# Kernel optimization log

Measured on AMD Instinct MI355X. Metric: run time of the kernel, lower is better.

The kernel has to match this reference:

```python
import jax, jax.numpy as jnp
import numpy as np

B, S, F, DK = 4, 2048, 1024, 1024

def setup_inputs() -> dict:
    key = jax.random.key(0)
    ks = jax.random.split(key, 9)
    sF = 1.0 / np.sqrt(F)
    sD = 1.0 / np.sqrt(DK)
    return {
        "x":  jax.random.normal(ks[0], (B, S, F), dtype=jnp.float32),
        "Wq": jax.random.normal(ks[1], (DK, F), dtype=jnp.float32) * sF,
        "bq": jax.random.normal(ks[2], (DK,), dtype=jnp.float32) * sF,
        "Wk": jax.random.normal(ks[3], (DK, F), dtype=jnp.float32) * sF,
        "bk": jax.random.normal(ks[4], (DK,), dtype=jnp.float32) * sF,
        "Wv": jax.random.normal(ks[5], (DK, F), dtype=jnp.float32) * sF,
        "bv": jax.random.normal(ks[6], (DK,), dtype=jnp.float32) * sF,
        "Wo": jax.random.normal(ks[7], (F, DK), dtype=jnp.float32) * sD,
        "bo": jax.random.normal(ks[8], (F,), dtype=jnp.float32) * sD,
    }

def reference(x, Wq, bq, Wk, bk, Wv, bv, Wo, bo):
    # Linear layers (torch convention: y = x @ W.T + b)
    q = jnp.einsum('bsf,df->bsd', x, Wq) + bq  # (B,S,DK)
    k = jnp.einsum('bsf,df->bsd', x, Wk) + bk  # (B,S,DK)
    v = jnp.einsum('bsf,df->bsd', x, Wv) + bv  # (B,S,DK)
    scale = 1.0 / (q.shape[-1] ** 0.5)
    scores = jnp.einsum('bqd,bkd->bqk', q, k) * scale  # (B,Sq,Sk)
    # Faithful to original: softmax over dim=-2 (the QUERY axis)
    attn = jax.nn.softmax(scores, axis=-2)
    ctx = jnp.einsum('bqk,bkd->bqd', attn, v)  # (B,S,DK)
    out = jnp.einsum('bsd,fd->bsf', ctx, Wo) + bo  # (B,S,F)
    return out
```

## Files before the change

### kernel.cpp

```cpp
#include <hip/hip_runtime.h>
#include <hip/hip_bf16.h>
#include <math.h>

typedef __bf16 bf16_t;
typedef __bf16 bf16x8 __attribute__((ext_vector_type(8)));
typedef float f32x4 __attribute__((ext_vector_type(4)));


__device__ __forceinline__ void g2l16(const bf16_t* g, bf16_t* l) {
  __builtin_amdgcn_global_load_lds(
      (const __attribute__((address_space(1))) void*)g,
      (__attribute__((address_space(3))) void*)l, 16, 0, 0);
}

__device__ __forceinline__ float waveMax(float v) {
#pragma unroll
  for (int o = 32; o > 0; o >>= 1) v = fmaxf(v, __shfl_xor(v, o));
  return v;
}
__device__ __forceinline__ float waveSum(float v) {
#pragma unroll
  for (int o = 32; o > 0; o >>= 1) v += __shfl_xor(v, o);
  return v;
}


__global__ __launch_bounds__(256) void cast_f32_to_bf16(
    const float* __restrict__ in, bf16_t* __restrict__ out, long n) {
  long i = ((long)blockIdx.x * 256 + threadIdx.x) * 8;
  if (i >= n) return;
  float4 a = *reinterpret_cast<const float4*>(in + i);
  float4 b = *reinterpret_cast<const float4*>(in + i + 4);
  bf16x8 o;
  o[0] = (bf16_t)a.x; o[1] = (bf16_t)a.y; o[2] = (bf16_t)a.z; o[3] = (bf16_t)a.w;
  o[4] = (bf16_t)b.x; o[5] = (bf16_t)b.y; o[6] = (bf16_t)b.z; o[7] = (bf16_t)b.w;
  *reinterpret_cast<bf16x8*>(out + i) = o;
}


template <int OUT_BF16, int HAS_BIAS>
__launch_bounds__(256, 2)
__global__ void gemm_bt(const bf16_t* __restrict__ A, const bf16_t* __restrict__ B,
                        const float* __restrict__ bias, void* __restrict__ Cv,
                        int M, int N, int K, float alpha,
                        long sA, long sB, long sC) {
  const bf16_t* Ab = A + (long)blockIdx.z * sA;
  const bf16_t* Bb = B + (long)blockIdx.z * sB;
  const int bm = blockIdx.x * 128;
  const int bn = blockIdx.y * 128;

  __shared__ bf16_t sAt[128 * 32];
  __shared__ bf16_t sBt[128 * 32];

  const int tid = threadIdx.x;
  const int lane = tid & 63;
  const int w = tid >> 6;
  const int wr = (w >> 1) * 64;
  const int wc = (w & 1) * 64;

  f32x4 acc[4][4] = {};

  const int r0 = tid >> 2;
  const int c0 = (tid & 3) * 8;
  const int r1 = 64 + (tid >> 2);
  const long lds0 = (long)tid * 8;
  const long lds1 = 2048 + (long)tid * 8;

  const int arow = wr + (lane & 15);
  const int brow = wc + (lane & 15);
  const int koff = (lane >> 4) * 8;

  const int nK = K >> 5;
  for (int kt = 0; kt < nK; ++kt) {
    const int k0 = kt << 5;
    g2l16(Ab + (long)(bm + r0) * K + k0 + c0, sAt + lds0);
    g2l16(Ab + (long)(bm + r1) * K + k0 + c0, sAt + lds1);
    g2l16(Bb + (long)(bn + r0) * K + k0 + c0, sBt + lds0);
    g2l16(Bb + (long)(bn + r1) * K + k0 + c0, sBt + lds1);
    __syncthreads();

    bf16x8 af[4], bfr[4];
#pragma unroll
    for (int m = 0; m < 4; ++m)
      af[m] = *reinterpret_cast<const bf16x8*>(sAt + (arow + m * 16) * 32 + koff);
#pragma unroll
    for (int n = 0; n < 4; ++n)
      bfr[n] = *reinterpret_cast<const bf16x8*>(sBt + (brow + n * 16) * 32 + koff);
#pragma unroll
    for (int m = 0; m < 4; ++m)
#pragma unroll
      for (int n = 0; n < 4; ++n)
        acc[m][n] = __builtin_amdgcn_mfma_f32_16x16x32_bf16(af[m], bfr[n], acc[m][n], 0, 0, 0);
    __syncthreads();
  }

  const int rbase = bm + wr + (lane >> 4) * 4;
  const int cbase = bn + wc + (lane & 15);
#pragma unroll
  for (int n = 0; n < 4; ++n) {
    const int col = cbase + n * 16;
    float bv = 0.f;
    if (HAS_BIAS) bv = bias[col];
#pragma unroll
    for (int m = 0; m < 4; ++m) {
      const int row0 = rbase + m * 16;
#pragma unroll
      for (int j = 0; j < 4; ++j) {
        float v = acc[m][n][j] * alpha + bv;
        if (OUT_BF16) {
          bf16_t* C = (bf16_t*)Cv + (long)blockIdx.z * sC;
          C[(long)(row0 + j) * N + col] = (bf16_t)v;
        } else {
          float* C = (float*)Cv + (long)blockIdx.z * sC;
          C[(long)(row0 + j) * N + col] = v;
        }
      }
    }
  }
}


__global__ __launch_bounds__(256) void row_stats(const float* __restrict__ S,
                                                 float* __restrict__ rmax,
                                                 float* __restrict__ rinv) {
  const long row = blockIdx.x;
  const float* p = S + row * 2048;
  const int t = threadIdx.x;
  float4 a = *reinterpret_cast<const float4*>(p + t * 8);
  float4 b = *reinterpret_cast<const float4*>(p + t * 8 + 4);
  float m = fmaxf(fmaxf(fmaxf(a.x, a.y), fmaxf(a.z, a.w)),
                  fmaxf(fmaxf(b.x, b.y), fmaxf(b.z, b.w)));
  m = waveMax(m);
  __shared__ float red[4];
  __shared__ float red2[4];
  if ((t & 63) == 0) red[t >> 6] = m;
  __syncthreads();
  m = fmaxf(fmaxf(red[0], red[1]), fmaxf(red[2], red[3]));
  float s = expf(a.x - m) + expf(a.y - m) + expf(a.z - m) + expf(a.w - m) +
            expf(b.x - m) + expf(b.y - m) + expf(b.z - m) + expf(b.w - m);
  s = waveSum(s);
  if ((t & 63) == 0) red2[t >> 6] = s;
  __syncthreads();
  s = red2[0] + red2[1] + red2[2] + red2[3];
  if (t == 0) { rmax[row] = m; rinv[row] = 1.0f / s; }
}


__global__ __launch_bounds__(256) void softmax_T(const float* __restrict__ S,
                                                 const float* __restrict__ rmax,
                                                 const float* __restrict__ rinv,
                                                 bf16_t* __restrict__ attn) {
  const int b = blockIdx.z;
  const int q0 = blockIdx.x * 64;
  const int kk0 = blockIdx.y * 64;
  __shared__ bf16_t tile[64][72];
  const int t = threadIdx.x;
  const int i = t >> 2;
  const int qj = (t & 3) * 16;
  const long grow = (long)b * 2048 + kk0 + i;
  const float mx = rmax[grow];
  const float ri = rinv[grow];
  const float* src = S + grow * 2048 + q0 + qj;
#pragma unroll
  for (int u = 0; u < 4; ++u) {
    float4 v = *reinterpret_cast<const float4*>(src + u * 4);
    tile[i][qj + u * 4 + 0] = (bf16_t)(expf(v.x - mx) * ri);
    tile[i][qj + u * 4 + 1] = (bf16_t)(expf(v.y - mx) * ri);
    tile[i][qj + u * 4 + 2] = (bf16_t)(expf(v.z - mx) * ri);
    tile[i][qj + u * 4 + 3] = (bf16_t)(expf(v.w - mx) * ri);
  }
  __syncthreads();
  const int j = t >> 2;
  const int kc = (t & 3) * 16;
  bf16x8 o0, o1;
#pragma unroll
  for (int u = 0; u < 8; ++u) o0[u] = tile[kc + u][j];
#pragma unroll
  for (int u = 0; u < 8; ++u) o1[u] = tile[kc + 8 + u][j];
  bf16_t* dst = attn + ((long)b * 2048 + q0 + j) * 2048 + kk0 + kc;
  *reinterpret_cast<bf16x8*>(dst) = o0;
  *reinterpret_cast<bf16x8*>(dst + 8) = o1;
}


__global__ __launch_bounds__(256) void transpose_bf16k(const bf16_t* __restrict__ in,
                                                       bf16_t* __restrict__ out,
                                                       int R, int C) {
  const int b = blockIdx.z;
  const int r0 = blockIdx.x * 64;
  const int c0 = blockIdx.y * 64;
  __shared__ bf16_t tile[64][72];
  const int t = threadIdx.x;
  const int i = t >> 2;
  const int cj = (t & 3) * 16;
  const bf16_t* src = in + ((long)b * R + r0 + i) * C + c0 + cj;
  bf16x8 a0 = *reinterpret_cast<const bf16x8*>(src);
  bf16x8 a1 = *reinterpret_cast<const bf16x8*>(src + 8);
#pragma unroll
  for (int u = 0; u < 8; ++u) { tile[i][cj + u] = a0[u]; tile[i][cj + 8 + u] = a1[u]; }
  __syncthreads();
  const int j = t >> 2;
  const int rc = (t & 3) * 16;
  bf16x8 o0, o1;
#pragma unroll
  for (int u = 0; u < 8; ++u) o0[u] = tile[rc + u][j];
#pragma unroll
  for (int u = 0; u < 8; ++u) o1[u] = tile[rc + 8 + u][j];
  bf16_t* dst = out + ((long)b * C + c0 + j) * R + r0 + rc;
  *reinterpret_cast<bf16x8*>(dst) = o0;
  *reinterpret_cast<bf16x8*>(dst + 8) = o1;
}


extern "C" void kernel_launch(void* const* d_in, const int* in_sizes, int n_in,
                              void* d_out, int out_size, void* d_ws, size_t ws_size,
                              hipStream_t stream) {
  const float* x  = (const float*)d_in[0];
  const float* Wq = (const float*)d_in[1];
  const float* bq = (const float*)d_in[2];
  const float* Wk = (const float*)d_in[3];
  const float* bk = (const float*)d_in[4];
  const float* Wv = (const float*)d_in[5];
  const float* bv = (const float*)d_in[6];
  const float* Wo = (const float*)d_in[7];
  const float* bo = (const float*)d_in[8];
  float* out = (float*)d_out;
  char* ws = (char*)d_ws;

  const long MB = 1024L * 1024L;
  bf16_t* xb   = (bf16_t*)(ws + 0);
  bf16_t* Wqb  = (bf16_t*)(ws + 16 * MB);
  bf16_t* Wkb  = (bf16_t*)(ws + 18 * MB);
  bf16_t* Wvb  = (bf16_t*)(ws + 20 * MB);
  bf16_t* Wob  = (bf16_t*)(ws + 22 * MB);
  bf16_t* Qb   = (bf16_t*)(ws + 24 * MB);
  bf16_t* Kb   = (bf16_t*)(ws + 40 * MB);
  bf16_t* Vb   = (bf16_t*)(ws + 56 * MB);
  float*  ST   = (float*)(ws + 72 * MB);
  bf16_t* attn = (bf16_t*)(ws + 136 * MB);
  float*  rmax = (float*)(ws + 168 * MB);
  float*  rinv = (float*)(ws + 168 * MB + 32768);
  bf16_t* VT   = (bf16_t*)(ws + 0);
  bf16_t* ctxb = (bf16_t*)(ws + 24 * MB);

  cast_f32_to_bf16<<<4096, 256, 0, stream>>>(x, xb, 8388608);
  cast_f32_to_bf16<<<512, 256, 0, stream>>>(Wq, Wqb, 1048576);
  cast_f32_to_bf16<<<512, 256, 0, stream>>>(Wk, Wkb, 1048576);
  cast_f32_to_bf16<<<512, 256, 0, stream>>>(Wv, Wvb, 1048576);
  cast_f32_to_bf16<<<512, 256, 0, stream>>>(Wo, Wob, 1048576);

  dim3 gqkv(64, 8, 1);
  gemm_bt<1, 1><<<gqkv, 256, 0, stream>>>(xb, Wqb, bq, Qb, 8192, 1024, 1024, 1.0f, 0, 0, 0);
  gemm_bt<1, 1><<<gqkv, 256, 0, stream>>>(xb, Wkb, bk, Kb, 8192, 1024, 1024, 1.0f, 0, 0, 0);
  gemm_bt<1, 1><<<gqkv, 256, 0, stream>>>(xb, Wvb, bv, Vb, 8192, 1024, 1024, 1.0f, 0, 0, 0);

  dim3 gst(16, 16, 4);
  gemm_bt<0, 0><<<gst, 256, 0, stream>>>(Kb, Qb, nullptr, ST, 2048, 2048, 1024, 0.03125f,
                                         2048L * 1024, 2048L * 1024, 2048L * 2048);

  row_stats<<<8192, 256, 0, stream>>>(ST, rmax, rinv);
  dim3 gsm(32, 32, 4);
  softmax_T<<<gsm, 256, 0, stream>>>(ST, rmax, rinv, attn);

  dim3 gtr(32, 16, 4);
  transpose_bf16k<<<gtr, 256, 0, stream>>>(Vb, VT, 2048, 1024);

  dim3 gctx(16, 8, 4);
  gemm_bt<1, 0><<<gctx, 256, 0, stream>>>(attn, VT, nullptr, ctxb, 2048, 1024, 2048, 1.0f,
                                          2048L * 2048, 1024L * 2048, 2048L * 1024);

  gemm_bt<0, 1><<<gqkv, 256, 0, stream>>>(ctxb, Wob, bo, out, 8192, 1024, 1024, 1.0f, 0, 0, 0);

  (void)in_sizes; (void)n_in; (void)out_size; (void)ws_size;
}
```

Measured before the change: 357.5 us.

## Add 256x256 pipelined MFMA GEMM and fuse QKV projections into one launch

Introduces a 512-thread GEMM kernel with 256x256 tiles, a double-buffered LDS pipeline filled by direct global-to-LDS loads, an XOR-swizzled LDS layout and explicit barrier/priority scheduling around 16x16x32 bf16 MFMA blocks. The Q, K and V weights are cast into one contiguous buffer so the three projections run as a single GEMM with N=3072, and the epilogue routes each column to the matching output and bias. The K*Q^T score GEMM also uses the new kernel. The aim is more data reuse per tile, fewer launches and better overlap of loads with MFMA, at the cost of high register pressure and a rigid hand-written schedule that assumes K is a multiple of 128.

New measurement: 335.0 us. 6.3% less time.

```diff
diff --git a/kernel.cpp b/kernel.cpp
--- a/kernel.cpp
+++ b/kernel.cpp
@@ -22,6 +22,12 @@
 #pragma unroll
   for (int o = 32; o > 0; o >>= 1) v += __shfl_xor(v, o);
   return v;
+}
+
+__device__ __forceinline__ bf16x8 rdf(const char* base, int row, int kbyte) {
+  int off = (row << 7) + kbyte;
+  off ^= (row & 7) << 4;
+  return *reinterpret_cast<const bf16x8*>(base + off);
 }
 
 
@@ -35,6 +41,185 @@
   o[0] = (bf16_t)a.x; o[1] = (bf16_t)a.y; o[2] = (bf16_t)a.z; o[3] = (bf16_t)a.w;
   o[4] = (bf16_t)b.x; o[5] = (bf16_t)b.y; o[6] = (bf16_t)b.z; o[7] = (bf16_t)b.w;
   *reinterpret_cast<bf16x8*>(out + i) = o;
+}
+
+
+#define MFMA_ ____nope
+
+#define STAGE256(d, o, h, t) do {                                              \
+  const bf16_t* gsrc_ = ((o) ? Bb : Ab) + (long)((h) * 128 + srl) * K +        \
+                        (long)(t) * 64 + sgsw;                                 \
+  bf16_t* ldsb_ = &lds[d][o][(h) * 8192] + ldst;                               \
+  g2l16(gsrc_, ldsb_);                                                         \
+  g2l16(gsrc_ + 64L * K, ldsb_ + 4096);                                        \
+} while (0)
+
+#define AREAD256(d, qm) do {                                                   \
+  const char* Ab_ = (const char*)&lds[d][0][0];                                \
+  int r_ = (qm) * 128 + wr2 * 64 + rA;                                         \
+  a0 = rdf(Ab_, r_, kb);      a1 = rdf(Ab_, r_, kb + 64);                      \
+  a2 = rdf(Ab_, r_ + 16, kb); a3 = rdf(Ab_, r_ + 16, kb + 64);                 \
+  a4 = rdf(Ab_, r_ + 32, kb); a5 = rdf(Ab_, r_ + 32, kb + 64);                 \
+  a6 = rdf(Ab_, r_ + 48, kb); a7 = rdf(Ab_, r_ + 48, kb + 64);                 \
+} while (0)
+
+#define BREAD256(d, qn, r0v, r1v, r2v, r3v) do {                               \
+  const char* Bb_ = (const char*)&lds[d][1][0];                                \
+  int c_ = (qn) * 128 + wc2 * 32 + rA;                                         \
+  r0v = rdf(Bb_, c_, kb);      r1v = rdf(Bb_, c_, kb + 64);                    \
+  r2v = rdf(Bb_, c_ + 16, kb); r3v = rdf(Bb_, c_ + 16, kb + 64);               \
+} while (0)
+
+#define MFMA16(qm, qn, b0v, b1v, b2v, b3v) do {                                \
+  acc[(qm)*4+0][(qn)*2+0] = __builtin_amdgcn_mfma_f32_16x16x32_bf16(a0, b0v, acc[(qm)*4+0][(qn)*2+0], 0,0,0); \
+  acc[(qm)*4+0][(qn)*2+0] = __builtin_amdgcn_mfma_f32_16x16x32_bf16(a1, b1v, acc[(qm)*4+0][(qn)*2+0], 0,0,0); \
+  acc[(qm)*4+1][(qn)*2+0] = __builtin_amdgcn_mfma_f32_16x16x32_bf16(a2, b0v, acc[(qm)*4+1][(qn)*2+0], 0,0,0); \
+  acc[(qm)*4+1][(qn)*2+0] = __builtin_amdgcn_mfma_f32_16x16x32_bf16(a3, b1v, acc[(qm)*4+1][(qn)*2+0], 0,0,0); \
+  acc[(qm)*4+2][(qn)*2+0] = __builtin_amdgcn_mfma_f32_16x16x32_bf16(a4, b0v, acc[(qm)*4+2][(qn)*2+0], 0,0,0); \
+  acc[(qm)*4+2][(qn)*2+0] = __builtin_amdgcn_mfma_f32_16x16x32_bf16(a5, b1v, acc[(qm)*4+2][(qn)*2+0], 0,0,0); \
+  acc[(qm)*4+3][(qn)*2+0] = __builtin_amdgcn_mfma_f32_16x16x32_bf16(a6, b0v, acc[(qm)*4+3][(qn)*2+0], 0,0,0); \
+  acc[(qm)*4+3][(qn)*2+0] = __builtin_amdgcn_mfma_f32_16x16x32_bf16(a7, b1v, acc[(qm)*4+3][(qn)*2+0], 0,0,0); \
+  acc[(qm)*4+0][(qn)*2+1] = __builtin_amdgcn_mfma_f32_16x16x32_bf16(a0, b2v, acc[(qm)*4+0][(qn)*2+1], 0,0,0); \
+  acc[(qm)*4+0][(qn)*2+1] = __builtin_amdgcn_mfma_f32_16x16x32_bf16(a1, b3v, acc[(qm)*4+0][(qn)*2+1], 0,0,0); \
+  acc[(qm)*4+1][(qn)*2+1] = __builtin_amdgcn_mfma_f32_16x16x32_bf16(a2, b2v, acc[(qm)*4+1][(qn)*2+1], 0,0,0); \
+  acc[(qm)*4+1][(qn)*2+1] = __builtin_amdgcn_mfma_f32_16x16x32_bf16(a3, b3v, acc[(qm)*4+1][(qn)*2+1], 0,0,0); \
+  acc[(qm)*4+2][(qn)*2+1] = __builtin_amdgcn_mfma_f32_16x16x32_bf16(a4, b2v, acc[(qm)*4+2][(qn)*2+1], 0,0,0); \
+  acc[(qm)*4+2][(qn)*2+1] = __builtin_amdgcn_mfma_f32_16x16x32_bf16(a5, b3v, acc[(qm)*4+2][(qn)*2+1], 0,0,0); \
+  acc[(qm)*4+3][(qn)*2+1] = __builtin_amdgcn_mfma_f32_16x16x32_bf16(a6, b2v, acc[(qm)*4+3][(qn)*2+1], 0,0,0); \
+  acc[(qm)*4+3][(qn)*2+1] = __builtin_amdgcn_mfma_f32_16x16x32_bf16(a7, b3v, acc[(qm)*4+3][(qn)*2+1], 0,0,0); \
+} while (0)
+
+#define PH_ENTER() do {                                                        \
+  __builtin_amdgcn_s_barrier();                                                \
+  asm volatile("s_waitcnt lgkmcnt(0)" ::: "memory");                           \
+  __builtin_amdgcn_sched_barrier(0);                                           \
+  __builtin_amdgcn_s_setprio(1);                                               \
+} while (0)
+
+#define PH_EXIT() do {                                                         \
+  __builtin_amdgcn_s_setprio(0);                                               \
+  __builtin_amdgcn_s_barrier();                                                \
+  __builtin_amdgcn_sched_barrier(0);                                           \
+} while (0)
+
+template <int EPI>
+__launch_bounds__(512, 2)
+__global__ void gemm256(const bf16_t* __restrict__ A, const bf16_t* __restrict__ B,
+                        int K, float alpha,
+                        void* __restrict__ C0, void* __restrict__ C1, void* __restrict__ C2,
+                        const float* __restrict__ bias0, const float* __restrict__ bias1,
+                        const float* __restrict__ bias2,
+                        int Ncols, long sA, long sB, long sC) {
+  __shared__ bf16_t lds[2][2][16384];
+
+  const int tid = threadIdx.x;
+  const int lane = tid & 63;
+  const int w = tid >> 6;
+  const int wr2 = w >> 2;
+  const int wc2 = w & 3;
+  const int rA = lane & 15;
+  const int kb = (lane >> 4) << 4;
+
+  const int bm = blockIdx.x * 256;
+  const int bn = blockIdx.y * 256;
+  const bf16_t* Ab = A + (long)blockIdx.z * sA + (long)bm * K;
+  const bf16_t* Bb = B + (long)blockIdx.z * sB + (long)bn * K;
+
+  const int srl = tid >> 3;
+  const int sgr = tid & 7;
+  const int sgsw = (sgr ^ (srl & 7)) * 8;
+  const int ldst = srl * 64 + sgr * 8;
+
+  f32x4 acc[8][4] = {};
+  bf16x8 a0, a1, a2, a3, a4, a5, a6, a7;
+  bf16x8 p0, p1, p2, p3, q0, q1, q2, q3;
+
+  const int NT = K >> 6;
+
+  STAGE256(0, 0, 0, 0); STAGE256(0, 1, 0, 0);
+  STAGE256(0, 0, 1, 0); STAGE256(0, 1, 1, 0);
+  STAGE256(1, 0, 0, 1); STAGE256(1, 1, 0, 1);
+  asm volatile("s_waitcnt vmcnt(4)" ::: "memory");
+  __builtin_amdgcn_s_barrier();
+  __builtin_amdgcn_sched_barrier(0);
+
+  int t = 0;
+  for (int it = 0; it < NT / 2 - 1; ++it, t += 2) {
+    AREAD256(0, 0); BREAD256(0, 0, p0, p1, p2, p3);
+    STAGE256(1, 0, 1, t + 1);
+    PH_ENTER(); MFMA16(0, 0, p0, p1, p2, p3); PH_EXIT();
+    BREAD256(0, 1, q0, q1, q2, q3);
+    STAGE256(1, 1, 1, t + 1);
+    PH_ENTER(); MFMA16(0, 1, q0, q1, q2, q3); PH_EXIT();
+    AREAD256(0, 1);
+    STAGE256(0, 0, 0, t + 2);
+    PH_ENTER(); MFMA16(1, 0, p0, p1, p2, p3); PH_EXIT();
+    STAGE256(0, 1, 0, t + 2);
+    asm volatile("s_waitcnt vmcnt(4)" ::: "memory");
+    PH_ENTER(); MFMA16(1, 1, q0, q1, q2, q3); PH_EXIT();
+    AREAD256(1, 0); BREAD256(1, 0, p0, p1, p2, p3);
+    STAGE256(0, 0, 1, t + 2);
+    PH_ENTER(); MFMA16(0, 0, p0, p1, p2, p3); PH_EXIT();
+    BREAD256(1, 1, q0, q1, q2, q3);
+    STAGE256(0, 1, 1, t + 2);
+    PH_ENTER(); MFMA16(0, 1, q0, q1, q2, q3); PH_EXIT();
+    AREAD256(1, 1);
+    STAGE256(1, 0, 0, t + 3);
+    PH_ENTER(); MFMA16(1, 0, p0, p1, p2, p3); PH_EXIT();
+    STAGE256(1, 1, 0, t + 3);
+    asm volatile("s_waitcnt vmcnt(4)" ::: "memory");
+    PH_ENTER(); MFMA16(1, 1, q0, q1, q2, q3); PH_EXIT();
+  }
+
+  AREAD256(0, 0); BREAD256(0, 0, p0, p1, p2, p3);
+  STAGE256(1, 0, 1, t + 1);
+  PH_ENTER(); MFMA16(0, 0, p0, p1, p2, p3); PH_EXIT();
+  BREAD256(0, 1, q0, q1, q2, q3);
+  STAGE256(1, 1, 1, t + 1);
+  PH_ENTER(); MFMA16(0, 1, q0, q1, q2, q3); PH_EXIT();
+  AREAD256(0, 1);
+  PH_ENTER(); MFMA16(1, 0, p0, p1, p2, p3); PH_EXIT();
+  asm volatile("s_waitcnt vmcnt(0)" ::: "memory");
+  PH_ENTER(); MFMA16(1, 1, q0, q1, q2, q3); PH_EXIT();
+  AREAD256(1, 0); BREAD256(1, 0, p0, p1, p2, p3);
+  PH_ENTER(); MFMA16(0, 0, p0, p1, p2, p3); PH_EXIT();
+  BREAD256(1, 1, q0, q1, q2, q3);
+  PH_ENTER(); MFMA16(0, 1, q0, q1, q2, q3); PH_EXIT();
+  AREAD256(1, 1);
+  PH_ENTER(); MFMA16(1, 0, p0, p1, p2, p3); PH_EXIT();
+  PH_ENTER(); MFMA16(1, 1, q0, q1, q2, q3); PH_EXIT();
+
+  const int rr = (lane >> 4) * 4;
+  const int cc = lane & 15;
+#pragma unroll
+  for (int qm = 0; qm < 2; ++qm)
+#pragma unroll
+    for (int m = 0; m < 4; ++m) {
+      const int grow = bm + qm * 128 + wr2 * 64 + m * 16 + rr;
+#pragma unroll
+      for (int qn = 0; qn < 2; ++qn)
+#pragma unroll
+        for (int n = 0; n < 2; ++n) {
+          const int gcol = bn + qn * 128 + wc2 * 32 + n * 16 + cc;
+          const f32x4 v = acc[qm * 4 + m][qn * 2 + n];
+          if (EPI == 0) {
+            float* C = (float*)C0 + (long)blockIdx.z * sC;
+#pragma unroll
+            for (int j = 0; j < 4; ++j)
+              C[(long)(grow + j) * Ncols + gcol] = v[j] * alpha;
+          } else {
+            const int sel = gcol >> 10;
+            const int lcol = gcol & 1023;
+            const float* bp = sel == 0 ? bias0 : (sel == 1 ? bias1 : bias2);
+            bf16_t* op = sel == 0 ? (bf16_t*)C0 : (sel == 1 ? (bf16_t*)C1 : (bf16_t*)C2);
+            const float bv = bp[lcol];
+#pragma unroll
+            for (int j = 0; j < 4; ++j)
+              op[(long)(grow + j) * 1024 + lcol] = (bf16_t)(v[j] + bv);
+          }
+        }
+    }
+  (void)Ncols;
 }
 
 
@@ -145,7 +330,6 @@
   if (t == 0) { rmax[row] = m; rinv[row] = 1.0f / s; }
 }
 
-
 __global__ __launch_bounds__(256) void softmax_T(const float* __restrict__ S,
                                                  const float* __restrict__ rmax,
                                                  const float* __restrict__ rinv,
@@ -182,7 +366,6 @@
   *reinterpret_cast<bf16x8*>(dst + 8) = o1;
 }
 
-
 __global__ __launch_bounds__(256) void transpose_bf16k(const bf16_t* __restrict__ in,
                                                        bf16_t* __restrict__ out,
                                                        int R, int C) {
@@ -228,35 +411,31 @@
   char* ws = (char*)d_ws;
 
   const long MB = 1024L * 1024L;
-  bf16_t* xb   = (bf16_t*)(ws + 0);
-  bf16_t* Wqb  = (bf16_t*)(ws + 16 * MB);
-  bf16_t* Wkb  = (bf16_t*)(ws + 18 * MB);
-  bf16_t* Wvb  = (bf16_t*)(ws + 20 * MB);
-  bf16_t* Wob  = (bf16_t*)(ws + 22 * MB);
-  bf16_t* Qb   = (bf16_t*)(ws + 24 * MB);
-  bf16_t* Kb   = (bf16_t*)(ws + 40 * MB);
-  bf16_t* Vb   = (bf16_t*)(ws + 56 * MB);
-  float*  ST   = (float*)(ws + 72 * MB);
-  bf16_t* attn = (bf16_t*)(ws + 136 * MB);
-  float*  rmax = (float*)(ws + 168 * MB);
-  float*  rinv = (float*)(ws + 168 * MB + 32768);
-  bf16_t* VT   = (bf16_t*)(ws + 0);
-  bf16_t* ctxb = (bf16_t*)(ws + 24 * MB);
+  bf16_t* xb    = (bf16_t*)(ws + 0);
+  bf16_t* Wqkvb = (bf16_t*)(ws + 16 * MB);
+  bf16_t* Wob   = (bf16_t*)(ws + 22 * MB);
+  bf16_t* Qb    = (bf16_t*)(ws + 24 * MB);
+  bf16_t* Kb    = (bf16_t*)(ws + 40 * MB);
+  bf16_t* Vb    = (bf16_t*)(ws + 56 * MB);
+  float*  ST    = (float*)(ws + 72 * MB);
+  bf16_t* attn  = (bf16_t*)(ws + 136 * MB);
+  float*  rmax  = (float*)(ws + 168 * MB);
+  float*  rinv  = (float*)(ws + 168 * MB + 32768);
+  bf16_t* VT    = (bf16_t*)(ws + 0);
+  bf16_t* ctxb  = (bf16_t*)(ws + 24 * MB);
 
   cast_f32_to_bf16<<<4096, 256, 0, stream>>>(x, xb, 8388608);
-  cast_f32_to_bf16<<<512, 256, 0, stream>>>(Wq, Wqb, 1048576);
-  cast_f32_to_bf16<<<512, 256, 0, stream>>>(Wk, Wkb, 1048576);
-  cast_f32_to_bf16<<<512, 256, 0, stream>>>(Wv, Wvb, 1048576);
+  cast_f32_to_bf16<<<512, 256, 0, stream>>>(Wq, Wqkvb, 1048576);
+  cast_f32_to_bf16<<<512, 256, 0, stream>>>(Wk, Wqkvb + 1048576, 1048576);
+  cast_f32_to_bf16<<<512, 256, 0, stream>>>(Wv, Wqkvb + 2097152, 1048576);
   cast_f32_to_bf16<<<512, 256, 0, stream>>>(Wo, Wob, 1048576);
 
-  dim3 gqkv(64, 8, 1);
-  gemm_bt<1, 1><<<gqkv, 256, 0, stream>>>(xb, Wqb, bq, Qb, 8192, 1024, 1024, 1.0f, 0, 0, 0);
-  gemm_bt<1, 1><<<gqkv, 256, 0, stream>>>(xb, Wkb, bk, Kb, 8192, 1024, 1024, 1.0f, 0, 0, 0);
-  gemm_bt<1, 1><<<gqkv, 256, 0, stream>>>(xb, Wvb, bv, Vb, 8192, 1024, 1024, 1.0f, 0, 0, 0);
-
-  dim3 gst(16, 16, 4);
-  gemm_bt<0, 0><<<gst, 256, 0, stream>>>(Kb, Qb, nullptr, ST, 2048, 2048, 1024, 0.03125f,
-                                         2048L * 1024, 2048L * 1024, 2048L * 2048);
+  gemm256<1><<<dim3(32, 12, 1), 512, 0, stream>>>(
+      xb, Wqkvb, 1024, 1.0f, Qb, Kb, Vb, bq, bk, bv, 3072, 0, 0, 0);
+
+  gemm256<0><<<dim3(8, 8, 4), 512, 0, stream>>>(
+      Kb, Qb, 1024, 0.03125f, ST, nullptr, nullptr, nullptr, nullptr, nullptr,
+      2048, 2048L * 1024, 2048L * 1024, 2048L * 2048);
 
   row_stats<<<8192, 256, 0, stream>>>(ST, rmax, rinv);
   dim3 gsm(32, 32, 4);
@@ -269,7 +448,8 @@
   gemm_bt<1, 0><<<gctx, 256, 0, stream>>>(attn, VT, nullptr, ctxb, 2048, 1024, 2048, 1.0f,
                                           2048L * 2048, 1024L * 2048, 2048L * 1024);
 
-  gemm_bt<0, 1><<<gqkv, 256, 0, stream>>>(ctxb, Wob, bo, out, 8192, 1024, 1024, 1.0f, 0, 0, 0);
+  dim3 gout(64, 8, 1);
+  gemm_bt<0, 1><<<gout, 256, 0, stream>>>(ctxb, Wob, bo, out, 8192, 1024, 1024, 1.0f, 0, 0, 0);
 
   (void)in_sizes; (void)n_in; (void)out_size; (void)ws_size;
 }
```
